# Kernel tuning notes

Hardware: AMD Instinct MI355X
Metric: run time of the kernel (lower is better)

The kernel has to match this reference:

```python
import jax, jax.numpy as jnp
import numpy as np

D_MODEL = 1024
NUM_HEADS = 4
KEY_DIM = 1024      # expand_k = 1
VALUE_DIM = 2048    # expand_v = 2
HEAD_QK = KEY_DIM // NUM_HEADS   # 256
HEAD_V = VALUE_DIM // NUM_HEADS  # 512
EPS = 1e-5
CHUNK = 64
ROPE_BASE = 10000.0


def apply_rotary(q, k):
    # q, k: (b, n, h, d), non-interleaved (rotate-half) rotary
    n, d = q.shape[1], q.shape[-1]
    inv_freq = 1.0 / (ROPE_BASE ** (jnp.arange(0, d, 2, dtype=jnp.float32) / d))
    t = jnp.arange(n, dtype=jnp.float32)
    freqs = jnp.outer(t, inv_freq)                     # (n, d/2)
    cos = jnp.cos(freqs)[None, :, None, :]
    sin = jnp.sin(freqs)[None, :, None, :]
    def rot(x):
        x1, x2 = jnp.split(x, 2, axis=-1)
        return jnp.concatenate([x1 * cos - x2 * sin, x2 * cos + x1 * sin], axis=-1)
    return rot(q), rot(k)


def chunk_retention(q, k, v, gamma, chunk=CHUNK):
    # q,k: (B,H,N,dk); v: (B,H,N,dv); gamma: (H,) per-head decay
    B, H, N, dk = q.shape
    dv = v.shape[-1]
    NC = N // chunk
    # (NC, B, H, C, d) chunked layout for scan
    qc = jnp.moveaxis(q.reshape(B, H, NC, chunk, dk), 2, 0)
    kc = jnp.moveaxis(k.reshape(B, H, NC, chunk, dk), 2, 0)
    vc = jnp.moveaxis(v.reshape(B, H, NC, chunk, dv), 2, 0)

    idx = jnp.arange(chunk)
    rel = idx[:, None] - idx[None, :]                       # i - j
    # intra-chunk decay mask D[h,i,j] = gamma_h**(i-j) for i>=j else 0
    D = jnp.where(rel >= 0, gamma[:, None, None] ** rel, 0.0)       # (H,C,C)
    cross_q = (gamma[:, None] ** (idx + 1))[None, :, :, None]       # (1,H,C,1)
    cross_k = (gamma[:, None] ** (chunk - 1 - idx))[None, :, :, None]
    gC = (gamma ** chunk)[None, :, None, None]                      # (1,H,1,1)

    def step(S, qkv):
        qb, kb, vb = qkv                                    # (B,H,C,d)
        attn = jnp.einsum('bhid,bhjd->bhij', qb, kb) * D[None]
        o_intra = jnp.einsum('bhij,bhjd->bhid', attn, vb)
        o_inter = jnp.einsum('bhid,bhde->bhie', qb * cross_q, S)
        S_new = gC * S + jnp.einsum('bhjd,bhje->bhde', kb * cross_k, vb)
        return S_new, o_intra + o_inter

    S0 = jnp.zeros((B, H, dk, dv), dtype=q.dtype)
    _, o = jax.lax.scan(step, S0, (qc, kc, vc))             # (NC,B,H,C,dv)
    return jnp.moveaxis(o, 0, 2).reshape(B, H, N, dv)


def rmsnorm(x, w):
    var = jnp.mean(x * x, axis=-1, keepdims=True)
    return x * jax.lax.rsqrt(var + EPS) * w


def setup_inputs() -> dict:
    key = jax.random.key(0)
    ks = jax.random.split(key, 7)
    B, N = 2, 4096
    s = 0.02
    return {
        'x': jax.random.normal(ks[0], (B, N, D_MODEL), dtype=jnp.float32),
        'Wq': jax.random.normal(ks[1], (D_MODEL, D_MODEL), dtype=jnp.float32) * s,
        'Wk': jax.random.normal(ks[2], (D_MODEL, D_MODEL), dtype=jnp.float32) * s,
        'Wv': jax.random.normal(ks[3], (D_MODEL, VALUE_DIM), dtype=jnp.float32) * s,
        'Wg': jax.random.normal(ks[4], (D_MODEL, VALUE_DIM), dtype=jnp.float32) * s,
        'Wo': jax.random.normal(ks[5], (VALUE_DIM, D_MODEL), dtype=jnp.float32) * s,
        'gn_weight': jnp.ones((HEAD_V,), dtype=jnp.float32),
    }


def reference(x, Wq, Wk, Wv, Wg, Wo, gn_weight):
    B, N, _ = x.shape
    H = NUM_HEADS
    q1 = (x @ Wq).reshape(B, N, H, HEAD_QK)
    k1 = (x @ Wk).reshape(B, N, H, HEAD_QK)
    q1, k1 = apply_rotary(q1, k1)
    q = jnp.transpose(q1, (0, 2, 1, 3)) * (HEAD_QK ** -0.5)   # (B,H,N,dk)
    k = jnp.transpose(k1, (0, 2, 1, 3))
    v = jnp.transpose((x @ Wv).reshape(B, N, H, HEAD_V), (0, 2, 1, 3))
    gamma = 1.0 - jnp.exp2(-5.0 - jnp.arange(H, dtype=jnp.float32))
    o = chunk_retention(q, k, v, gamma)                       # (B,H,N,dv_h)
    o = jnp.transpose(o, (0, 2, 1, 3))                        # (B,N,H,dv_h)
    o = rmsnorm(o, gn_weight)
    g = jax.nn.silu(x @ Wg)                                   # (B,N,VALUE_DIM)
    o = o.reshape(B, N, VALUE_DIM) * g
    return o @ Wo
```

## Files before the change

kernel.cpp:

```cpp
#include <hip/hip_runtime.h>

#define NS   4096
#define NBAT 2
#define NH   4
#define DKH  256
#define DVH  512
#define DM   1024
#define VD   2048
#define CH   64
#define NCH  64

typedef unsigned short u16;
typedef unsigned int   u32;

using bf16x8 = __attribute__((ext_vector_type(8))) short;
using f32x4  = __attribute__((ext_vector_type(4))) float;

__device__ __forceinline__ float bf2f(u16 a) {
  return __uint_as_float(((u32)a) << 16);
}
__device__ __forceinline__ u16 f2bf(float f) {
  u32 u = __float_as_uint(f);
  u32 r = (u + 0x7fffu + ((u >> 16) & 1u)) >> 16;
  return (u16)r;
}
__device__ __forceinline__ void unpack2(u32 v, float& lo, float& hi) {
  lo = __uint_as_float(v << 16);
  hi = __uint_as_float(v & 0xffff0000u);
}
__device__ __forceinline__ void unpack8(uint4 v, float* f) {
  unpack2(v.x, f[0], f[1]); unpack2(v.y, f[2], f[3]);
  unpack2(v.z, f[4], f[5]); unpack2(v.w, f[6], f[7]);
}

__device__ __forceinline__ void gl_lds16(const u16* g, u16* l) {
  __builtin_amdgcn_global_load_lds(
      (const __attribute__((address_space(1))) void*)g,
      (__attribute__((address_space(3))) void*)l,
      16, 0, 0);
}

__global__ __launch_bounds__(256) void cvt_bf16(const float* __restrict__ X,
                                                u16* __restrict__ Y) {
  size_t t = (size_t)blockIdx.x * 256 + threadIdx.x;
  float4 v = *(const float4*)(X + t * 4);
  ushort4 o;
  o.x = f2bf(v.x); o.y = f2bf(v.y); o.z = f2bf(v.z); o.w = f2bf(v.w);
  *(ushort4*)(Y + t * 4) = o;
}

__global__ __launch_bounds__(256) void transpose_bf16(const float* __restrict__ W,
                                                      u16* __restrict__ Wt,
                                                      int K, int N) {
  __shared__ float tile[64][65];
  const int n0 = blockIdx.x * 64, k0 = blockIdx.y * 64;
  const int t = threadIdx.x;
  const int r = t >> 4, c = (t & 15) << 2;
#pragma unroll
  for (int it = 0; it < 4; it++) {
    float4 v = *(const float4*)(W + (size_t)(k0 + r + it * 16) * N + n0 + c);
    tile[r + it * 16][c + 0] = v.x; tile[r + it * 16][c + 1] = v.y;
    tile[r + it * 16][c + 2] = v.z; tile[r + it * 16][c + 3] = v.w;
  }
  __syncthreads();
#pragma unroll
  for (int it = 0; it < 4; it++) {
    const int nr = r + it * 16;
    ushort4 o;
    o.x = f2bf(tile[c + 0][nr]); o.y = f2bf(tile[c + 1][nr]);
    o.z = f2bf(tile[c + 2][nr]); o.w = f2bf(tile[c + 3][nr]);
    *(ushort4*)(Wt + (size_t)(n0 + nr) * K + k0 + c) = o;
  }
}

template<bool OBF>
__global__ __launch_bounds__(256) void gemm_mfma(const u16* __restrict__ A,
                                                 const u16* __restrict__ Bt,
                                                 void* __restrict__ C,
                                                 int M, int N, int K) {
  __shared__ u16 sA[128 * 64];
  __shared__ u16 sB[128 * 64];
  const int tid = threadIdx.x;
  const int wave = tid >> 6, lane = tid & 63;
  const int wm = (wave >> 1) << 6;
  const int wn = (wave & 1) << 6;
  const int row0 = blockIdx.y << 7, col0 = blockIdx.x << 7;

  const int srow = tid >> 3;
  const int sk   = (tid & 7) << 3;

  const u16* aRow = A + (size_t)(row0 + srow) * K + sk;
  const u16* bRow = Bt + (size_t)(col0 + srow) * K + sk;
  u16* sAp = sA + tid * 8;
  u16* sBp = sB + tid * 8;

  f32x4 acc[4][4] = {};

  const int fm = lane & 15;
  const int fk = (lane >> 4) << 3;
  const u16* sAf = sA + (wm + fm) * 64 + fk;
  const u16* sBf = sB + (wn + fm) * 64 + fk;

  for (int k0 = 0; k0 < K; k0 += 64) {
#pragma unroll
    for (int it = 0; it < 4; it++) {
      gl_lds16(aRow + (size_t)(it * 32) * K + k0, sAp + it * 2048);
      gl_lds16(bRow + (size_t)(it * 32) * K + k0, sBp + it * 2048);
    }
    __syncthreads();
#pragma unroll
    for (int kk = 0; kk < 64; kk += 32) {
      bf16x8 af[4], bfr[4];
#pragma unroll
      for (int mt = 0; mt < 4; mt++) af[mt] = *(const bf16x8*)(sAf + mt * 1024 + kk);
#pragma unroll
      for (int nt = 0; nt < 4; nt++) bfr[nt] = *(const bf16x8*)(sBf + nt * 1024 + kk);
#pragma unroll
      for (int mt = 0; mt < 4; mt++)
#pragma unroll
        for (int nt = 0; nt < 4; nt++)
          acc[mt][nt] = __builtin_amdgcn_mfma_f32_16x16x32_bf16(af[mt], bfr[nt], acc[mt][nt], 0, 0, 0);
    }
    __syncthreads();
  }

  const int er = lane >> 4;
  const int ec = lane & 15;
#pragma unroll
  for (int mt = 0; mt < 4; mt++) {
#pragma unroll
    for (int nt = 0; nt < 4; nt++) {
#pragma unroll
      for (int r = 0; r < 4; r++) {
        const size_t row = (size_t)row0 + wm + mt * 16 + er * 4 + r;
        const size_t col = (size_t)col0 + wn + nt * 16 + ec;
        if constexpr (OBF) ((u16*)C)[row * N + col] = f2bf(acc[mt][nt][r]);
        else               ((float*)C)[row * N + col] = acc[mt][nt][r];
      }
    }
  }
}

__global__ __launch_bounds__(256) void rope_kernel(u16* __restrict__ Q, u16* __restrict__ K) {
  size_t t = (size_t)blockIdx.x * 256 + threadIdx.x;
  int j = (int)(t & 127);
  int h = (int)((t >> 7) & 3);
  size_t bn = t >> 9;
  int n = (int)(bn & (NS - 1));
  float ang = (float)n * exp2f(-(float)j * (13.2877123795494f / 128.0f));
  float s, c;
  sincosf(ang, &s, &c);
  size_t base = bn * DM + (size_t)h * DKH + j;
  const float sc = 0.0625f;
  float q1 = bf2f(Q[base]), q2 = bf2f(Q[base + 128]);
  Q[base]       = f2bf((q1 * c - q2 * s) * sc);
  Q[base + 128] = f2bf((q2 * c + q1 * s) * sc);
  float k1 = bf2f(K[base]), k2 = bf2f(K[base + 128]);
  K[base]       = f2bf(k1 * c - k2 * s);
  K[base + 128] = f2bf(k2 * c + k1 * s);
}

__global__ __launch_bounds__(256) void transpose_k(const u16* __restrict__ Kb,
                                                   u16* __restrict__ KT) {
  __shared__ u16 tile[64][68];
  const int wg = blockIdx.x;
  const int dt = wg & 3, nt = (wg >> 2) & 63, h = (wg >> 8) & 3, b = wg >> 10;
  const int tid = threadIdx.x;
  const int r = tid >> 2, cb = (tid & 3) << 4;
  const u16* src = Kb + (size_t)(b * NS + nt * 64 + r) * DM + h * DKH + dt * 64 + cb;
  *(uint4*)&tile[r][cb]     = *(const uint4*)(src);
  *(uint4*)&tile[r][cb + 8] = *(const uint4*)(src + 8);
  __syncthreads();
  const int dr = tid >> 2, ncb = (tid & 3) << 4;
  u32 w[8];
#pragma unroll
  for (int u = 0; u < 8; u++)
    w[u] = (u32)tile[ncb + 2 * u][dr] | ((u32)tile[ncb + 2 * u + 1][dr] << 16);
  u16* dst = KT + ((size_t)((b * NH + h) * 256) + dt * 64 + dr) * NS + nt * 64 + ncb;
  *(uint4*)(dst)     = make_uint4(w[0], w[1], w[2], w[3]);
  *(uint4*)(dst + 8) = make_uint4(w[4], w[5], w[6], w[7]);
}

__global__ __launch_bounds__(256) void attn_mfma(const u16* __restrict__ Q,
                                                 const u16* __restrict__ Kb,
                                                 u16* __restrict__ At) {
  __shared__ u16 sQ[64][264];
  __shared__ u16 sK[64][264];
  const int wg = blockIdx.x;
  const int c = wg & 63, h = (wg >> 6) & 3, b = wg >> 8;
  const int n0 = c << 6;
  const int tid = threadIdx.x;
  const int wave = tid >> 6, lane = tid & 63;
  const int quad = lane >> 4, col = lane & 15;
  {
    const int r = tid >> 2, cb = (tid & 3) << 6;
    const u16* qsrc = Q  + (size_t)(b * NS + n0 + r) * DM + h * DKH + cb;
    const u16* ksrc = Kb + (size_t)(b * NS + n0 + r) * DM + h * DKH + cb;
#pragma unroll
    for (int u = 0; u < 8; u++) {
      *(uint4*)&sQ[r][cb + u * 8] = *(const uint4*)(qsrc + u * 8);
      *(uint4*)&sK[r][cb + u * 8] = *(const uint4*)(ksrc + u * 8);
    }
  }
  __syncthreads();
  const int i0 = wave << 4;
  f32x4 acc[4] = {};
#pragma unroll
  for (int ks = 0; ks < 256; ks += 32) {
    bf16x8 a = *(const bf16x8*)&sQ[i0 + col][ks + quad * 8];
#pragma unroll
    for (int nt = 0; nt < 4; nt++) {
      bf16x8 bb = *(const bf16x8*)&sK[nt * 16 + col][ks + quad * 8];
      acc[nt] = __builtin_amdgcn_mfma_f32_16x16x32_bf16(a, bb, acc[nt], 0, 0, 0);
    }
  }
  const float l2g = log2f(1.0f - exp2f(-5.0f - (float)h));
  u16* dst = At + ((size_t)wg << 12);
#pragma unroll
  for (int nt = 0; nt < 4; nt++) {
    int j = nt * 16 + col;
#pragma unroll
    for (int rr = 0; rr < 4; rr++) {
      int i = i0 + quad * 4 + rr;
      int rel = i - j;
      float v = (rel >= 0) ? acc[nt][rr] * exp2f((float)rel * l2g) : 0.0f;
      dst[i * 64 + j] = f2bf(v);
    }
  }
}

__global__ __launch_bounds__(256) void scan_mfma(const u16* __restrict__ Q,
                                                 const u16* __restrict__ KT,
                                                 const u16* __restrict__ At,
                                                 u16* V) {
  __shared__ u16 sQ[64][264];
  __shared__ u16 sKT[256][72];
  __shared__ u16 sAi[64][72];
  __shared__ u16 sVT[32][72];
  __shared__ u16 sVkT[32][72];
  __shared__ u16 sSb[32][264];

  const int wg = blockIdx.x;
  const int es = wg & 15, h = (wg >> 4) & 3, b = wg >> 6;
  const int tid = threadIdx.x;
  const int wave = tid >> 6, lane = tid & 63;
  const int quad = lane >> 4, col = lane & 15;

  const float gamma = 1.0f - exp2f(-5.0f - (float)h);
  const float l2g = log2f(gamma);
  const float gC = exp2f(64.0f * l2g);

  const int qr = tid >> 2, qc = (tid & 3) << 6;
  const int ar = tid >> 2, ac = (tid & 3) << 4;
  const int vj = tid >> 2, ve = (tid & 3) << 3;
  const float ckj = exp2f((float)(63 - vj) * l2g);

  const int i0 = wave << 4;
  const int d0w = wave << 6;
  const float cq_base = exp2f((float)(i0 + quad * 4 + 1) * l2g);

  const u16* Qbase  = Q + ((size_t)b * NS) * DM + h * DKH;
  const u16* KTbase = KT + ((size_t)(b * NH + h) * 256) * NS;
  const u16* Atbase = At + ((size_t)((b * NH + h) * NCH) << 12);
  u16* Vbase = V + ((size_t)b * NS) * VD + h * DVH + es * 32;

  f32x4 accU[4][2] = {};

  for (int ch = 0; ch < NCH; ch++) {
    const int n0 = ch << 6;
    {
      const u16* src = Qbase + (size_t)(n0 + qr) * DM + qc;
#pragma unroll
      for (int u = 0; u < 8; u++)
        *(uint4*)&sQ[qr][qc + u * 8] = *(const uint4*)(src + u * 8);
    }
#pragma unroll
    for (int u = 0; u < 8; u++) {
      int cc = u * 256 + tid;
      int d = cc >> 3, off = (cc & 7) << 3;
      *(uint4*)&sKT[d][off] = *(const uint4*)(KTbase + (size_t)d * NS + n0 + off);
    }
    {
      const u16* src = Atbase + ((size_t)ch << 12) + ar * 64 + ac;
      *(uint4*)&sAi[ar][ac]     = *(const uint4*)(src);
      *(uint4*)&sAi[ar][ac + 8] = *(const uint4*)(src + 8);
    }
    {
      uint4 vv = *(const uint4*)(Vbase + (size_t)(n0 + vj) * VD + ve);
      float vf[8]; unpack8(vv, vf);
      const u16* raw = (const u16*)&vv;
#pragma unroll
      for (int u = 0; u < 8; u++) {
        sVT[ve + u][vj]  = raw[u];
        sVkT[ve + u][vj] = f2bf(vf[u] * ckj);
      }
    }
    __syncthreads();

    {
      f32x4 ai[2] = {}, ae[2] = {};
#pragma unroll
      for (int ks = 0; ks < 64; ks += 32) {
        bf16x8 a = *(const bf16x8*)&sAi[i0 + col][ks + quad * 8];
#pragma unroll
        for (int nt = 0; nt < 2; nt++) {
          bf16x8 bb = *(const bf16x8*)&sVT[nt * 16 + col][ks + quad * 8];
          ai[nt] = __builtin_amdgcn_mfma_f32_16x16x32_bf16(a, bb, ai[nt], 0, 0, 0);
        }
      }
      if (ch) {
#pragma unroll
        for (int ks = 0; ks < 256; ks += 32) {
          bf16x8 a = *(const bf16x8*)&sQ[i0 + col][ks + quad * 8];
#pragma unroll
          for (int nt = 0; nt < 2; nt++) {
            bf16x8 bb = *(const bf16x8*)&sSb[nt * 16 + col][ks + quad * 8];
            ae[nt] = __builtin_amdgcn_mfma_f32_16x16x32_bf16(a, bb, ae[nt], 0, 0, 0);
          }
        }
      }
      float cq = cq_base;
#pragma unroll
      for (int r = 0; r < 4; r++) {
        int i = i0 + quad * 4 + r;
        u16* dst = Vbase + (size_t)(n0 + i) * VD + col;
#pragma unroll
        for (int nt = 0; nt < 2; nt++)
          dst[nt * 16] = f2bf(ai[nt][r] + cq * ae[nt][r]);
        cq *= gamma;
      }
    }

#pragma unroll
    for (int mt = 0; mt < 4; mt++)
#pragma unroll
      for (int nt = 0; nt < 2; nt++)
        accU[mt][nt] = accU[mt][nt] * gC;
#pragma unroll
    for (int ks = 0; ks < 64; ks += 32) {
      bf16x8 bb[2];
#pragma unroll
      for (int nt = 0; nt < 2; nt++)
        bb[nt] = *(const bf16x8*)&sVkT[nt * 16 + col][ks + quad * 8];
#pragma unroll
      for (int mt = 0; mt < 4; mt++) {
        bf16x8 a = *(const bf16x8*)&sKT[d0w + mt * 16 + col][ks + quad * 8];
#pragma unroll
        for (int nt = 0; nt < 2; nt++)
          accU[mt][nt] = __builtin_amdgcn_mfma_f32_16x16x32_bf16(a, bb[nt], accU[mt][nt], 0, 0, 0);
      }
    }
    __syncthreads();

#pragma unroll
    for (int mt = 0; mt < 4; mt++) {
      int d = d0w + mt * 16 + quad * 4;
#pragma unroll
      for (int nt = 0; nt < 2; nt++) {
        int e = nt * 16 + col;
#pragma unroll
        for (int r = 0; r < 4; r++)
          sSb[e][d + r] = f2bf(accU[mt][nt][r]);
      }
    }
  }
}

__global__ __launch_bounds__(256) void norm_gate_kernel(const u16* __restrict__ O,
                                                        const u16* __restrict__ G,
                                                        const float* __restrict__ gnw,
                                                        u16* __restrict__ OG) {
  const int bn = blockIdx.x;
  const int wave = threadIdx.x >> 6;
  const int lane = threadIdx.x & 63;
  const size_t base = (size_t)bn * VD + (size_t)wave * DVH;
  float vals[8];
  float ss = 0.f;
#pragma unroll
  for (int k = 0; k < 8; k++) {
    float v = bf2f(O[base + lane + 64 * k]);
    vals[k] = v;
    ss += v * v;
  }
#pragma unroll
  for (int off = 32; off > 0; off >>= 1) ss += __shfl_xor(ss, off, 64);
  const float r = rsqrtf(ss * (1.0f / 512.0f) + 1e-5f);
#pragma unroll
  for (int k = 0; k < 8; k++) {
    int e = lane + 64 * k;
    float g = bf2f(G[base + e]);
    float sig = 1.0f / (1.0f + expf(-g));
    OG[base + e] = f2bf(vals[k] * r * gnw[e] * g * sig);
  }
}

extern "C" void kernel_launch(void* const* d_in, const int* in_sizes, int n_in,
                              void* d_out, int out_size, void* d_ws, size_t ws_size,
                              hipStream_t stream) {
  const float* x   = (const float*)d_in[0];
  const float* Wq  = (const float*)d_in[1];
  const float* Wk  = (const float*)d_in[2];
  const float* Wv  = (const float*)d_in[3];
  const float* Wg  = (const float*)d_in[4];
  const float* Wo  = (const float*)d_in[5];
  const float* gnw = (const float*)d_in[6];

  char* ws = (char*)d_ws;
  u16*   xb  = (u16*)(ws);
  u16*   Qb  = (u16*)(ws + (16u  << 20));
  u16*   Kb  = (u16*)(ws + (32u  << 20));
  u16*   Vb  = (u16*)(ws + (48u  << 20));
  u16*   Gb  = (u16*)(ws + (80u  << 20));
  u16*   At  = (u16*)(ws + (112u << 20));
  u16*   KTg = (u16*)(ws + (116u << 20));
  u16*   Wqt = (u16*)(ws + (132u << 20));
  u16*   Wkt = (u16*)(ws + (134u << 20));
  u16*   Wvt = (u16*)(ws + (136u << 20));
  u16*   Wgt = (u16*)(ws + (140u << 20));
  u16*   Wot = (u16*)(ws + (144u << 20));
  u16*   OG  = (u16*)(ws);

  dim3 blk(256);
  const int M = NBAT * NS;

  cvt_bf16<<<8192, blk, 0, stream>>>(x, xb);
  transpose_bf16<<<dim3(16, 16), blk, 0, stream>>>(Wq, Wqt, DM, DM);
  transpose_bf16<<<dim3(16, 16), blk, 0, stream>>>(Wk, Wkt, DM, DM);
  transpose_bf16<<<dim3(32, 16), blk, 0, stream>>>(Wv, Wvt, DM, VD);
  transpose_bf16<<<dim3(32, 16), blk, 0, stream>>>(Wg, Wgt, DM, VD);
  transpose_bf16<<<dim3(16, 32), blk, 0, stream>>>(Wo, Wot, VD, DM);

  gemm_mfma<true><<<dim3(8, 64),  blk, 0, stream>>>(xb, Wqt, Qb, M, DM, DM);
  gemm_mfma<true><<<dim3(8, 64),  blk, 0, stream>>>(xb, Wkt, Kb, M, DM, DM);
  gemm_mfma<true><<<dim3(16, 64), blk, 0, stream>>>(xb, Wvt, Vb, M, VD, DM);
  gemm_mfma<true><<<dim3(16, 64), blk, 0, stream>>>(xb, Wgt, Gb, M, VD, DM);

  rope_kernel<<<16384, blk, 0, stream>>>(Qb, Kb);
  transpose_k<<<2048, blk, 0, stream>>>(Kb, KTg);
  attn_mfma<<<512, blk, 0, stream>>>(Qb, Kb, At);
  scan_mfma<<<128, blk, 0, stream>>>(Qb, KTg, At, Vb);
  norm_gate_kernel<<<M, blk, 0, stream>>>(Vb, Gb, gnw, OG);

  gemm_mfma<false><<<dim3(8, 64), blk, 0, stream>>>(OG, Wot, (float*)d_out, M, DM, VD);
}
```

Before: 593.9 us.

## Split scan into output/state warp roles with register-prefetched chunk operands

The retention scan kernel is reorganized: value columns per block are halved so twice as many blocks launch, each with 512 threads, where four waves compute chunk outputs and four waves update the recurrent state. Q, intra-chunk attention and K^T tiles are loaded straight into registers and double-buffered for the next chunk instead of being staged through shared memory, which cuts LDS usage and overlaps global loads with MFMA work. This targets the low parallelism of the serial 64-chunk scan (only 128 blocks before) at the cost of more register pressure and duplicated Q/K loads across twice as many blocks.

Measured after the change: 550.8 us. 7.3% less time.

```diff
diff --git a/kernel.cpp b/kernel.cpp
--- a/kernel.cpp
+++ b/kernel.cpp
@@ -229,19 +229,16 @@
   }
 }
 
-__global__ __launch_bounds__(256) void scan_mfma(const u16* __restrict__ Q,
-                                                 const u16* __restrict__ KT,
-                                                 const u16* __restrict__ At,
-                                                 u16* V) {
-  __shared__ u16 sQ[64][264];
-  __shared__ u16 sKT[256][72];
-  __shared__ u16 sAi[64][72];
-  __shared__ u16 sVT[32][72];
-  __shared__ u16 sVkT[32][72];
-  __shared__ u16 sSb[32][264];
+__global__ __launch_bounds__(512, 2) void scan_mfma(const u16* __restrict__ Q,
+                                                    const u16* __restrict__ KT,
+                                                    const u16* __restrict__ At,
+                                                    u16* V) {
+  __shared__ u16 sVT[16][72];
+  __shared__ u16 sVkT[16][72];
+  __shared__ u16 sSb[16][264];
 
   const int wg = blockIdx.x;
-  const int es = wg & 15, h = (wg >> 4) & 3, b = wg >> 6;
+  const int es = wg & 31, h = (wg >> 5) & 3, b = wg >> 7;
   const int tid = threadIdx.x;
   const int wave = tid >> 6, lane = tid & 63;
   const int quad = lane >> 4, col = lane & 15;
@@ -250,45 +247,48 @@
   const float l2g = log2f(gamma);
   const float gC = exp2f(64.0f * l2g);
 
-  const int qr = tid >> 2, qc = (tid & 3) << 6;
-  const int ar = tid >> 2, ac = (tid & 3) << 4;
-  const int vj = tid >> 2, ve = (tid & 3) << 3;
+  const bool isO = wave < 4;
+  const int i0  = (wave & 3) << 4;
+  const int d0w = (wave & 3) << 6;
+  const float cq0 = exp2f((float)(i0 + quad * 4 + 1) * l2g);
+
+  const u16* Qb2 = Q  + (size_t)b * NS * DM + h * DKH;
+  const u16* KTb = KT + (size_t)((b * NH + h) * 256) * NS;
+  const u16* Atb = At + ((size_t)((b * NH + h) * NCH) << 12);
+  u16* Vb2 = V + (size_t)b * NS * VD + h * DVH + es * 16;
+
+  const int vj = (tid & 127) >> 1, ve = (tid & 1) << 3;
   const float ckj = exp2f((float)(63 - vj) * l2g);
 
-  const int i0 = wave << 4;
-  const int d0w = wave << 6;
-  const float cq_base = exp2f((float)(i0 + quad * 4 + 1) * l2g);
-
-  const u16* Qbase  = Q + ((size_t)b * NS) * DM + h * DKH;
-  const u16* KTbase = KT + ((size_t)(b * NH + h) * 256) * NS;
-  const u16* Atbase = At + ((size_t)((b * NH + h) * NCH) << 12);
-  u16* Vbase = V + ((size_t)b * NS) * VD + h * DVH + es * 32;
-
-  f32x4 accU[4][2] = {};
-
+  bf16x8 qf[2][8], af[2][2], kf[2][8];
+  uint4 vv[2];
+
+  if (tid < 128) vv[0] = *(const uint4*)(Vb2 + (size_t)vj * VD + ve);
+  if (isO) {
+    const u16* qrow = Qb2 + (size_t)(i0 + col) * DM + quad * 8;
+#pragma unroll
+    for (int k = 0; k < 8; k++) qf[0][k] = *(const bf16x8*)(qrow + k * 32);
+    const u16* arow = Atb + (i0 + col) * 64 + quad * 8;
+    af[0][0] = *(const bf16x8*)(arow);
+    af[0][1] = *(const bf16x8*)(arow + 32);
+  } else {
+#pragma unroll
+    for (int mt = 0; mt < 4; mt++) {
+      const u16* krow = KTb + (size_t)(d0w + mt * 16 + col) * NS + quad * 8;
+      kf[0][mt * 2]     = *(const bf16x8*)(krow);
+      kf[0][mt * 2 + 1] = *(const bf16x8*)(krow + 32);
+    }
+  }
+
+  f32x4 accU[4] = {};
+
+#pragma unroll 2
   for (int ch = 0; ch < NCH; ch++) {
+    const int cur = ch & 1, nxt = cur ^ 1;
     const int n0 = ch << 6;
-    {
-      const u16* src = Qbase + (size_t)(n0 + qr) * DM + qc;
-#pragma unroll
-      for (int u = 0; u < 8; u++)
-        *(uint4*)&sQ[qr][qc + u * 8] = *(const uint4*)(src + u * 8);
-    }
-#pragma unroll
-    for (int u = 0; u < 8; u++) {
-      int cc = u * 256 + tid;
-      int d = cc >> 3, off = (cc & 7) << 3;
-      *(uint4*)&sKT[d][off] = *(const uint4*)(KTbase + (size_t)d * NS + n0 + off);
-    }
-    {
-      const u16* src = Atbase + ((size_t)ch << 12) + ar * 64 + ac;
-      *(uint4*)&sAi[ar][ac]     = *(const uint4*)(src);
-      *(uint4*)&sAi[ar][ac + 8] = *(const uint4*)(src + 8);
-    }
-    {
-      uint4 vv = *(const uint4*)(Vbase + (size_t)(n0 + vj) * VD + ve);
-      float vf[8]; unpack8(vv, vf);
-      const u16* raw = (const u16*)&vv;
+    if (tid < 128) {
+      float vf[8]; unpack8(vv[cur], vf);
+      const u16* raw = (const u16*)&vv[cur];
 #pragma unroll
       for (int u = 0; u < 8; u++) {
         sVT[ve + u][vj]  = raw[u];
@@ -296,71 +296,65 @@
       }
     }
     __syncthreads();
-
-    {
-      f32x4 ai[2] = {}, ae[2] = {};
-#pragma unroll
-      for (int ks = 0; ks < 64; ks += 32) {
-        bf16x8 a = *(const bf16x8*)&sAi[i0 + col][ks + quad * 8];
-#pragma unroll
-        for (int nt = 0; nt < 2; nt++) {
-          bf16x8 bb = *(const bf16x8*)&sVT[nt * 16 + col][ks + quad * 8];
-          ai[nt] = __builtin_amdgcn_mfma_f32_16x16x32_bf16(a, bb, ai[nt], 0, 0, 0);
+    if (ch + 1 < NCH) {
+      const int n1 = n0 + 64;
+      if (tid < 128) vv[nxt] = *(const uint4*)(Vb2 + (size_t)(n1 + vj) * VD + ve);
+      if (isO) {
+        const u16* qrow = Qb2 + (size_t)(n1 + i0 + col) * DM + quad * 8;
+#pragma unroll
+        for (int k = 0; k < 8; k++) qf[nxt][k] = *(const bf16x8*)(qrow + k * 32);
+        const u16* arow = Atb + ((size_t)(ch + 1) << 12) + (i0 + col) * 64 + quad * 8;
+        af[nxt][0] = *(const bf16x8*)(arow);
+        af[nxt][1] = *(const bf16x8*)(arow + 32);
+      } else {
+#pragma unroll
+        for (int mt = 0; mt < 4; mt++) {
+          const u16* krow = KTb + (size_t)(d0w + mt * 16 + col) * NS + n1 + quad * 8;
+          kf[nxt][mt * 2]     = *(const bf16x8*)(krow);
+          kf[nxt][mt * 2 + 1] = *(const bf16x8*)(krow + 32);
         }
       }
+    }
+    if (isO) {
+      f32x4 ai = {}, ae = {};
+#pragma unroll
+      for (int k = 0; k < 2; k++) {
+        bf16x8 bb = *(const bf16x8*)&sVT[col][k * 32 + quad * 8];
+        ai = __builtin_amdgcn_mfma_f32_16x16x32_bf16(af[cur][k], bb, ai, 0, 0, 0);
+      }
       if (ch) {
 #pragma unroll
-        for (int ks = 0; ks < 256; ks += 32) {
-          bf16x8 a = *(const bf16x8*)&sQ[i0 + col][ks + quad * 8];
-#pragma unroll
-          for (int nt = 0; nt < 2; nt++) {
-            bf16x8 bb = *(const bf16x8*)&sSb[nt * 16 + col][ks + quad * 8];
-            ae[nt] = __builtin_amdgcn_mfma_f32_16x16x32_bf16(a, bb, ae[nt], 0, 0, 0);
-          }
+        for (int k = 0; k < 8; k++) {
+          bf16x8 bb = *(const bf16x8*)&sSb[col][k * 32 + quad * 8];
+          ae = __builtin_amdgcn_mfma_f32_16x16x32_bf16(qf[cur][k], bb, ae, 0, 0, 0);
         }
       }
-      float cq = cq_base;
+      float cq = cq0;
 #pragma unroll
       for (int r = 0; r < 4; r++) {
-        int i = i0 + quad * 4 + r;
-        u16* dst = Vbase + (size_t)(n0 + i) * VD + col;
-#pragma unroll
-        for (int nt = 0; nt < 2; nt++)
-          dst[nt * 16] = f2bf(ai[nt][r] + cq * ae[nt][r]);
+        u16* dst = Vb2 + (size_t)(n0 + i0 + quad * 4 + r) * VD + col;
+        *dst = f2bf(ai[r] + cq * ae[r]);
         cq *= gamma;
       }
-    }
-
-#pragma unroll
-    for (int mt = 0; mt < 4; mt++)
-#pragma unroll
-      for (int nt = 0; nt < 2; nt++)
-        accU[mt][nt] = accU[mt][nt] * gC;
-#pragma unroll
-    for (int ks = 0; ks < 64; ks += 32) {
-      bf16x8 bb[2];
-#pragma unroll
-      for (int nt = 0; nt < 2; nt++)
-        bb[nt] = *(const bf16x8*)&sVkT[nt * 16 + col][ks + quad * 8];
+    } else {
+#pragma unroll
+      for (int mt = 0; mt < 4; mt++) accU[mt] *= gC;
+#pragma unroll
+      for (int k = 0; k < 2; k++) {
+        bf16x8 bb = *(const bf16x8*)&sVkT[col][k * 32 + quad * 8];
+#pragma unroll
+        for (int mt = 0; mt < 4; mt++)
+          accU[mt] = __builtin_amdgcn_mfma_f32_16x16x32_bf16(kf[cur][mt * 2 + k], bb, accU[mt], 0, 0, 0);
+      }
+    }
+    __syncthreads();
+    if (!isO) {
 #pragma unroll
       for (int mt = 0; mt < 4; mt++) {
-        bf16x8 a = *(const bf16x8*)&sKT[d0w + mt * 16 + col][ks + quad * 8];
-#pragma unroll
-        for (int nt = 0; nt < 2; nt++)
-          accU[mt][nt] = __builtin_amdgcn_mfma_f32_16x16x32_bf16(a, bb[nt], accU[mt][nt], 0, 0, 0);
-      }
-    }
-    __syncthreads();
-
-#pragma unroll
-    for (int mt = 0; mt < 4; mt++) {
-      int d = d0w + mt * 16 + quad * 4;
-#pragma unroll
-      for (int nt = 0; nt < 2; nt++) {
-        int e = nt * 16 + col;
+        int d = d0w + mt * 16 + quad * 4;
 #pragma unroll
         for (int r = 0; r < 4; r++)
-          sSb[e][d + r] = f2bf(accU[mt][nt][r]);
+          sSb[col][d + r] = f2bf(accU[mt][r]);
       }
     }
   }
@@ -438,7 +432,7 @@
   rope_kernel<<<16384, blk, 0, stream>>>(Qb, Kb);
   transpose_k<<<2048, blk, 0, stream>>>(Kb, KTg);
   attn_mfma<<<512, blk, 0, stream>>>(Qb, Kb, At);
-  scan_mfma<<<128, blk, 0, stream>>>(Qb, KTg, At, Vb);
+  scan_mfma<<<256, dim3(512), 0, stream>>>(Qb, KTg, At, Vb);
   norm_gate_kernel<<<M, blk, 0, stream>>>(Vb, Gb, gnw, OG);
 
   gemm_mfma<false><<<dim3(8, 64), blk, 0, stream>>>(OG, Wot, (float*)d_out, M, DM, VD);
```

## Split chunk retention scan into parallel state pass and segmented output pass

Applied to the files above, without the earlier changes.

Replaces the single 128-block sequential scan with two kernels. A state pass computes inter-chunk states every 8 chunks across many small wavefront blocks. An output pass then processes 8 segments in parallel per head, seeded from those checkpoints, keeping the state in registers and using a 16x16x16 MFMA for the Q·S product. The V projection GEMM now writes V transposed so both passes read it directly. This targets the low parallelism of the serial scan, at the cost of extra state recompute, global checkpoint traffic, heavy register use, and uncoalesced global loads without LDS staging.

After: 668.8 us. +12.6%, slower.

```diff
diff --git a/kernel.cpp b/kernel.cpp
--- a/kernel.cpp
+++ b/kernel.cpp
@@ -9,11 +9,13 @@
 #define VD   2048
 #define CH   64
 #define NCH  64
+#define MROW (NBAT * NS)
 
 typedef unsigned short u16;
 typedef unsigned int   u32;
 
 using bf16x8 = __attribute__((ext_vector_type(8))) short;
+using bf16x4 = __attribute__((ext_vector_type(4))) short;
 using f32x4  = __attribute__((ext_vector_type(4))) float;
 
 __device__ __forceinline__ float bf2f(u16 a) {
@@ -38,6 +40,38 @@
       (const __attribute__((address_space(1))) void*)g,
       (__attribute__((address_space(3))) void*)l,
       16, 0, 0);
+}
+
+__device__ __forceinline__ f32x4 mfma32(bf16x8 a, bf16x8 b, f32x4 c) {
+  return __builtin_amdgcn_mfma_f32_16x16x32_bf16(a, b, c, 0, 0, 0);
+}
+
+__device__ __forceinline__ f32x4 mfma16(bf16x4 a, bf16x4 b, f32x4 c) {
+#if __has_builtin(__builtin_amdgcn_mfma_f32_16x16x16bf16_1k)
+  return __builtin_amdgcn_mfma_f32_16x16x16bf16_1k(a, b, c, 0, 0, 0);
+#else
+  asm("v_mfma_f32_16x16x16_bf16 %0, %1, %2, %0" : "+v"(c) : "v"(a), "v"(b));
+  return c;
+#endif
+}
+
+__device__ __forceinline__ bf16x8 scale8(bf16x8 v, const float* ckv) {
+  u32* w = (u32*)&v;
+  bf16x8 out;
+  u32* ow = (u32*)&out;
+#pragma unroll
+  for (int p = 0; p < 4; p++) {
+    float lo, hi; unpack2(w[p], lo, hi);
+    ow[p] = (u32)f2bf(lo * ckv[2 * p]) | ((u32)f2bf(hi * ckv[2 * p + 1]) << 16);
+  }
+  return out;
+}
+
+__device__ __forceinline__ bf16x4 pack4(f32x4 v) {
+  bf16x4 o;
+  o[0] = (short)f2bf(v[0]); o[1] = (short)f2bf(v[1]);
+  o[2] = (short)f2bf(v[2]); o[3] = (short)f2bf(v[3]);
+  return o;
 }
 
 __global__ __launch_bounds__(256) void cvt_bf16(const float* __restrict__ X,
@@ -73,7 +107,7 @@
   }
 }
 
-template<bool OBF>
+template<int OMODE>
 __global__ __launch_bounds__(256) void gemm_mfma(const u16* __restrict__ A,
                                                  const u16* __restrict__ Bt,
                                                  void* __restrict__ C,
@@ -119,7 +153,7 @@
       for (int mt = 0; mt < 4; mt++)
 #pragma unroll
         for (int nt = 0; nt < 4; nt++)
-          acc[mt][nt] = __builtin_amdgcn_mfma_f32_16x16x32_bf16(af[mt], bfr[nt], acc[mt][nt], 0, 0, 0);
+          acc[mt][nt] = mfma32(af[mt], bfr[nt], acc[mt][nt]);
     }
     __syncthreads();
   }
@@ -130,12 +164,21 @@
   for (int mt = 0; mt < 4; mt++) {
 #pragma unroll
     for (int nt = 0; nt < 4; nt++) {
-#pragma unroll
-      for (int r = 0; r < 4; r++) {
-        const size_t row = (size_t)row0 + wm + mt * 16 + er * 4 + r;
-        const size_t col = (size_t)col0 + wn + nt * 16 + ec;
-        if constexpr (OBF) ((u16*)C)[row * N + col] = f2bf(acc[mt][nt][r]);
-        else               ((float*)C)[row * N + col] = acc[mt][nt][r];
+      if constexpr (OMODE == 2) {
+        ushort4 o;
+        o.x = f2bf(acc[mt][nt][0]); o.y = f2bf(acc[mt][nt][1]);
+        o.z = f2bf(acc[mt][nt][2]); o.w = f2bf(acc[mt][nt][3]);
+        u16* dst = (u16*)C + (size_t)(col0 + wn + nt * 16 + ec) * M +
+                   row0 + wm + mt * 16 + er * 4;
+        *(ushort4*)dst = o;
+      } else {
+#pragma unroll
+        for (int r = 0; r < 4; r++) {
+          const size_t row = (size_t)row0 + wm + mt * 16 + er * 4 + r;
+          const size_t col = (size_t)col0 + wn + nt * 16 + ec;
+          if constexpr (OMODE == 1) ((u16*)C)[row * N + col] = f2bf(acc[mt][nt][r]);
+          else                      ((float*)C)[row * N + col] = acc[mt][nt][r];
+        }
       }
     }
   }
@@ -211,7 +254,7 @@
 #pragma unroll
     for (int nt = 0; nt < 4; nt++) {
       bf16x8 bb = *(const bf16x8*)&sK[nt * 16 + col][ks + quad * 8];
-      acc[nt] = __builtin_amdgcn_mfma_f32_16x16x32_bf16(a, bb, acc[nt], 0, 0, 0);
+      acc[nt] = mfma32(a, bb, acc[nt]);
     }
   }
   const float l2g = log2f(1.0f - exp2f(-5.0f - (float)h));
@@ -229,139 +272,192 @@
   }
 }
 
-__global__ __launch_bounds__(256) void scan_mfma(const u16* __restrict__ Q,
-                                                 const u16* __restrict__ KT,
-                                                 const u16* __restrict__ At,
-                                                 u16* V) {
-  __shared__ u16 sQ[64][264];
-  __shared__ u16 sKT[256][72];
-  __shared__ u16 sAi[64][72];
-  __shared__ u16 sVT[32][72];
-  __shared__ u16 sVkT[32][72];
-  __shared__ u16 sSb[32][264];
-
+__global__ __launch_bounds__(64) void state_pass(const u16* __restrict__ KT,
+                                                 const u16* __restrict__ VT,
+                                                 u16* __restrict__ Sc) {
   const int wg = blockIdx.x;
-  const int es = wg & 15, h = (wg >> 4) & 3, b = wg >> 6;
-  const int tid = threadIdx.x;
-  const int wave = tid >> 6, lane = tid & 63;
+  const int bh = wg & 7, slice = wg >> 3;
+  const int ds = slice & 7, es = slice >> 3;
+  const int b = bh >> 2, h = bh & 3;
+  const int lane = threadIdx.x;
   const int quad = lane >> 4, col = lane & 15;
-
   const float gamma = 1.0f - exp2f(-5.0f - (float)h);
   const float l2g = log2f(gamma);
   const float gC = exp2f(64.0f * l2g);
-
-  const int qr = tid >> 2, qc = (tid & 3) << 6;
-  const int ar = tid >> 2, ac = (tid & 3) << 4;
-  const int vj = tid >> 2, ve = (tid & 3) << 3;
-  const float ckj = exp2f((float)(63 - vj) * l2g);
-
-  const int i0 = wave << 4;
-  const int d0w = wave << 6;
-  const float cq_base = exp2f((float)(i0 + quad * 4 + 1) * l2g);
-
-  const u16* Qbase  = Q + ((size_t)b * NS) * DM + h * DKH;
-  const u16* KTbase = KT + ((size_t)(b * NH + h) * 256) * NS;
-  const u16* Atbase = At + ((size_t)((b * NH + h) * NCH) << 12);
-  u16* Vbase = V + ((size_t)b * NS) * VD + h * DVH + es * 32;
-
-  f32x4 accU[4][2] = {};
-
+  float ck[2][8];
+#pragma unroll
+  for (int ks = 0; ks < 2; ks++)
+#pragma unroll
+    for (int u = 0; u < 8; u++)
+      ck[ks][u] = exp2f((float)(63 - (ks * 32 + quad * 8 + u)) * l2g);
+
+  const u16* KTb = KT + (size_t)(bh * 256 + ds * 32) * NS;
+  const u16* vrow = VT + (size_t)(h * DVH + es * 16 + col) * MROW + (size_t)b * NS;
+
+  f32x4 S[2] = {};
+  bf16x8 kf[2][4], vf[2][2];
+
+#pragma unroll
+  for (int mt = 0; mt < 2; mt++)
+#pragma unroll
+    for (int ks = 0; ks < 2; ks++)
+      kf[0][mt * 2 + ks] = *(const bf16x8*)(KTb + (size_t)(mt * 16 + col) * NS + ks * 32 + quad * 8);
+#pragma unroll
+  for (int ks = 0; ks < 2; ks++)
+    vf[0][ks] = *(const bf16x8*)(vrow + ks * 32 + quad * 8);
+
+#pragma unroll 2
   for (int ch = 0; ch < NCH; ch++) {
+    const int cur = ch & 1, nxt = cur ^ 1;
+    if (ch + 1 < NCH) {
+      const int n1 = (ch + 1) << 6;
+#pragma unroll
+      for (int mt = 0; mt < 2; mt++)
+#pragma unroll
+        for (int ks = 0; ks < 2; ks++)
+          kf[nxt][mt * 2 + ks] = *(const bf16x8*)(KTb + (size_t)(mt * 16 + col) * NS + n1 + ks * 32 + quad * 8);
+#pragma unroll
+      for (int ks = 0; ks < 2; ks++)
+        vf[nxt][ks] = *(const bf16x8*)(vrow + n1 + ks * 32 + quad * 8);
+    }
+#pragma unroll
+    for (int mt = 0; mt < 2; mt++) S[mt] *= gC;
+#pragma unroll
+    for (int ks = 0; ks < 2; ks++) {
+      bf16x8 ckv = scale8(vf[cur][ks], ck[ks]);
+#pragma unroll
+      for (int mt = 0; mt < 2; mt++)
+        S[mt] = mfma32(kf[cur][mt * 2 + ks], ckv, S[mt]);
+    }
+    if ((ch & 7) == 7 && ch != NCH - 1) {
+      const int sidx = ch >> 3;
+      u16* sp = Sc + (size_t)((bh * 7 + sidx) * 512 + es * 16 + col) * 256 + ds * 32;
+#pragma unroll
+      for (int mt = 0; mt < 2; mt++) {
+        ushort4 o;
+        o.x = f2bf(S[mt][0]); o.y = f2bf(S[mt][1]);
+        o.z = f2bf(S[mt][2]); o.w = f2bf(S[mt][3]);
+        *(ushort4*)(sp + mt * 16 + quad * 4) = o;
+      }
+    }
+  }
+}
+
+__global__ __launch_bounds__(64, 1) void out_pass(const u16* __restrict__ Q,
+                                                  const u16* __restrict__ KT,
+                                                  const u16* __restrict__ At,
+                                                  const u16* __restrict__ VT,
+                                                  const u16* __restrict__ Sc,
+                                                  u16* __restrict__ O) {
+  const int wg = blockIdx.x;
+  const int grp = wg & 63, es = wg >> 6;
+  const int sc = grp & 7, bh = grp >> 3;
+  const int b = bh >> 2, h = bh & 3;
+  const int lane = threadIdx.x;
+  const int quad = lane >> 4, col = lane & 15;
+  const float gamma = 1.0f - exp2f(-5.0f - (float)h);
+  const float l2g = log2f(gamma);
+  const float gC = exp2f(64.0f * l2g);
+  const float g16 = exp2f(16.0f * l2g);
+  const float cq00 = exp2f((float)(quad * 4 + 1) * l2g);
+  float ck[2][8];
+#pragma unroll
+  for (int ks = 0; ks < 2; ks++)
+#pragma unroll
+    for (int u = 0; u < 8; u++)
+      ck[ks][u] = exp2f((float)(63 - (ks * 32 + quad * 8 + u)) * l2g);
+
+  const u16* Qb  = Q + (size_t)(b * NS) * DM + h * DKH;
+  const u16* KTb = KT + (size_t)(bh * 256) * NS;
+  const u16* Atb = At + ((size_t)(bh * NCH) << 12);
+  const u16* vrow0 = VT + (size_t)(h * DVH + es * 32 + col) * MROW + (size_t)b * NS;
+  const u16* vrow1 = vrow0 + (size_t)16 * MROW;
+  u16* Ob = O + (size_t)(b * NS) * VD + h * DVH + es * 32;
+
+  f32x4 S[2][16];
+  bf16x4 SB[2][16];
+  if (sc) {
+    const u16* sp0 = Sc + (size_t)((bh * 7 + sc - 1) * 512 + es * 32 + col) * 256;
+    const u16* sp1 = sp0 + (size_t)16 * 256;
+#pragma unroll
+    for (int mt = 0; mt < 16; mt++) {
+      ushort4 w0 = *(const ushort4*)(sp0 + mt * 16 + quad * 4);
+      ushort4 w1 = *(const ushort4*)(sp1 + mt * 16 + quad * 4);
+      SB[0][mt][0] = (short)w0.x; SB[0][mt][1] = (short)w0.y;
+      SB[0][mt][2] = (short)w0.z; SB[0][mt][3] = (short)w0.w;
+      SB[1][mt][0] = (short)w1.x; SB[1][mt][1] = (short)w1.y;
+      SB[1][mt][2] = (short)w1.z; SB[1][mt][3] = (short)w1.w;
+      S[0][mt] = f32x4{bf2f(w0.x), bf2f(w0.y), bf2f(w0.z), bf2f(w0.w)};
+      S[1][mt] = f32x4{bf2f(w1.x), bf2f(w1.y), bf2f(w1.z), bf2f(w1.w)};
+    }
+  } else {
+#pragma unroll
+    for (int nt = 0; nt < 2; nt++)
+#pragma unroll
+      for (int mt = 0; mt < 16; mt++) { S[nt][mt] = f32x4{0.f, 0.f, 0.f, 0.f}; SB[nt][mt] = bf16x4{0, 0, 0, 0}; }
+  }
+
+  for (int c = 0; c < 8; c++) {
+    const int ch = sc * 8 + c;
     const int n0 = ch << 6;
-    {
-      const u16* src = Qbase + (size_t)(n0 + qr) * DM + qc;
-#pragma unroll
-      for (int u = 0; u < 8; u++)
-        *(uint4*)&sQ[qr][qc + u * 8] = *(const uint4*)(src + u * 8);
-    }
-#pragma unroll
-    for (int u = 0; u < 8; u++) {
-      int cc = u * 256 + tid;
-      int d = cc >> 3, off = (cc & 7) << 3;
-      *(uint4*)&sKT[d][off] = *(const uint4*)(KTbase + (size_t)d * NS + n0 + off);
-    }
-    {
-      const u16* src = Atbase + ((size_t)ch << 12) + ar * 64 + ac;
-      *(uint4*)&sAi[ar][ac]     = *(const uint4*)(src);
-      *(uint4*)&sAi[ar][ac + 8] = *(const uint4*)(src + 8);
-    }
-    {
-      uint4 vv = *(const uint4*)(Vbase + (size_t)(n0 + vj) * VD + ve);
-      float vf[8]; unpack8(vv, vf);
-      const u16* raw = (const u16*)&vv;
-#pragma unroll
-      for (int u = 0; u < 8; u++) {
-        sVT[ve + u][vj]  = raw[u];
-        sVkT[ve + u][vj] = f2bf(vf[u] * ckj);
+    f32x4 ai[4][2] = {}, ae[4][2] = {};
+    bf16x8 vfr[2][2];
+#pragma unroll
+    for (int ks = 0; ks < 2; ks++) {
+      vfr[ks][0] = *(const bf16x8*)(vrow0 + n0 + ks * 32 + quad * 8);
+      vfr[ks][1] = *(const bf16x8*)(vrow1 + n0 + ks * 32 + quad * 8);
+#pragma unroll
+      for (int mt = 0; mt < 4; mt++) {
+        bf16x8 a = *(const bf16x8*)(Atb + ((size_t)ch << 12) + (mt * 16 + col) * 64 + ks * 32 + quad * 8);
+        ai[mt][0] = mfma32(a, vfr[ks][0], ai[mt][0]);
+        ai[mt][1] = mfma32(a, vfr[ks][1], ai[mt][1]);
       }
     }
-    __syncthreads();
-
-    {
-      f32x4 ai[2] = {}, ae[2] = {};
-#pragma unroll
-      for (int ks = 0; ks < 64; ks += 32) {
-        bf16x8 a = *(const bf16x8*)&sAi[i0 + col][ks + quad * 8];
-#pragma unroll
-        for (int nt = 0; nt < 2; nt++) {
-          bf16x8 bb = *(const bf16x8*)&sVT[nt * 16 + col][ks + quad * 8];
-          ai[nt] = __builtin_amdgcn_mfma_f32_16x16x32_bf16(a, bb, ai[nt], 0, 0, 0);
+    if (sc || c) {
+#pragma unroll
+      for (int kt = 0; kt < 16; kt++) {
+#pragma unroll
+        for (int mt = 0; mt < 4; mt++) {
+          ushort4 qa = *(const ushort4*)(Qb + (size_t)(n0 + mt * 16 + col) * DM + kt * 16 + quad * 4);
+          bf16x4 a; a[0] = (short)qa.x; a[1] = (short)qa.y; a[2] = (short)qa.z; a[3] = (short)qa.w;
+          ae[mt][0] = mfma16(a, SB[0][kt], ae[mt][0]);
+          ae[mt][1] = mfma16(a, SB[1][kt], ae[mt][1]);
         }
       }
-      if (ch) {
-#pragma unroll
-        for (int ks = 0; ks < 256; ks += 32) {
-          bf16x8 a = *(const bf16x8*)&sQ[i0 + col][ks + quad * 8];
-#pragma unroll
-          for (int nt = 0; nt < 2; nt++) {
-            bf16x8 bb = *(const bf16x8*)&sSb[nt * 16 + col][ks + quad * 8];
-            ae[nt] = __builtin_amdgcn_mfma_f32_16x16x32_bf16(a, bb, ae[nt], 0, 0, 0);
-          }
+    }
+    float cqr = cq00;
+#pragma unroll
+    for (int mt = 0; mt < 4; mt++) {
+      float cq = cqr;
+#pragma unroll
+      for (int r = 0; r < 4; r++) {
+        u16* dst = Ob + (size_t)(n0 + mt * 16 + quad * 4 + r) * VD;
+        dst[col]      = f2bf(ai[mt][0][r] + cq * ae[mt][0][r]);
+        dst[16 + col] = f2bf(ai[mt][1][r] + cq * ae[mt][1][r]);
+        cq *= gamma;
+      }
+      cqr *= g16;
+    }
+    if (c < 7) {
+#pragma unroll
+      for (int nt = 0; nt < 2; nt++)
+#pragma unroll
+        for (int mt = 0; mt < 16; mt++) S[nt][mt] *= gC;
+#pragma unroll
+      for (int ks = 0; ks < 2; ks++) {
+        bf16x8 ckv0 = scale8(vfr[ks][0], ck[ks]);
+        bf16x8 ckv1 = scale8(vfr[ks][1], ck[ks]);
+#pragma unroll
+        for (int mt = 0; mt < 16; mt++) {
+          bf16x8 a = *(const bf16x8*)(KTb + (size_t)(mt * 16 + col) * NS + n0 + ks * 32 + quad * 8);
+          S[0][mt] = mfma32(a, ckv0, S[0][mt]);
+          S[1][mt] = mfma32(a, ckv1, S[1][mt]);
         }
       }
-      float cq = cq_base;
-#pragma unroll
-      for (int r = 0; r < 4; r++) {
-        int i = i0 + quad * 4 + r;
-        u16* dst = Vbase + (size_t)(n0 + i) * VD + col;
-#pragma unroll
-        for (int nt = 0; nt < 2; nt++)
-          dst[nt * 16] = f2bf(ai[nt][r] + cq * ae[nt][r]);
-        cq *= gamma;
-      }
-    }
-
-#pragma unroll
-    for (int mt = 0; mt < 4; mt++)
 #pragma unroll
       for (int nt = 0; nt < 2; nt++)
-        accU[mt][nt] = accU[mt][nt] * gC;
-#pragma unroll
-    for (int ks = 0; ks < 64; ks += 32) {
-      bf16x8 bb[2];
-#pragma unroll
-      for (int nt = 0; nt < 2; nt++)
-        bb[nt] = *(const bf16x8*)&sVkT[nt * 16 + col][ks + quad * 8];
-#pragma unroll
-      for (int mt = 0; mt < 4; mt++) {
-        bf16x8 a = *(const bf16x8*)&sKT[d0w + mt * 16 + col][ks + quad * 8];
-#pragma unroll
-        for (int nt = 0; nt < 2; nt++)
-          accU[mt][nt] = __builtin_amdgcn_mfma_f32_16x16x32_bf16(a, bb[nt], accU[mt][nt], 0, 0, 0);
-      }
-    }
-    __syncthreads();
-
-#pragma unroll
-    for (int mt = 0; mt < 4; mt++) {
-      int d = d0w + mt * 16 + quad * 4;
-#pragma unroll
-      for (int nt = 0; nt < 2; nt++) {
-        int e = nt * 16 + col;
-#pragma unroll
-        for (int r = 0; r < 4; r++)
-          sSb[e][d + r] = f2bf(accU[mt][nt][r]);
-      }
+#pragma unroll
+        for (int mt = 0; mt < 16; mt++) SB[nt][mt] = pack4(S[nt][mt]);
     }
   }
 }
@@ -407,9 +503,10 @@
 
   char* ws = (char*)d_ws;
   u16*   xb  = (u16*)(ws);
+  u16*   Sc  = (u16*)(ws);
   u16*   Qb  = (u16*)(ws + (16u  << 20));
   u16*   Kb  = (u16*)(ws + (32u  << 20));
-  u16*   Vb  = (u16*)(ws + (48u  << 20));
+  u16*   VT  = (u16*)(ws + (48u  << 20));
   u16*   Gb  = (u16*)(ws + (80u  << 20));
   u16*   At  = (u16*)(ws + (112u << 20));
   u16*   KTg = (u16*)(ws + (116u << 20));
@@ -418,10 +515,11 @@
   u16*   Wvt = (u16*)(ws + (136u << 20));
   u16*   Wgt = (u16*)(ws + (140u << 20));
   u16*   Wot = (u16*)(ws + (144u << 20));
+  u16*   Ob  = (u16*)(ws + (148u << 20));
   u16*   OG  = (u16*)(ws);
 
   dim3 blk(256);
-  const int M = NBAT * NS;
+  const int M = MROW;
 
   cvt_bf16<<<8192, blk, 0, stream>>>(x, xb);
   transpose_bf16<<<dim3(16, 16), blk, 0, stream>>>(Wq, Wqt, DM, DM);
@@ -430,16 +528,18 @@
   transpose_bf16<<<dim3(32, 16), blk, 0, stream>>>(Wg, Wgt, DM, VD);
   transpose_bf16<<<dim3(16, 32), blk, 0, stream>>>(Wo, Wot, VD, DM);
 
-  gemm_mfma<true><<<dim3(8, 64),  blk, 0, stream>>>(xb, Wqt, Qb, M, DM, DM);
-  gemm_mfma<true><<<dim3(8, 64),  blk, 0, stream>>>(xb, Wkt, Kb, M, DM, DM);
-  gemm_mfma<true><<<dim3(16, 64), blk, 0, stream>>>(xb, Wvt, Vb, M, VD, DM);
-  gemm_mfma<true><<<dim3(16, 64), blk, 0, stream>>>(xb, Wgt, Gb, M, VD, DM);
+  gemm_mfma<1><<<dim3(8, 64),  blk, 0, stream>>>(xb, Wqt, Qb, M, DM, DM);
+  gemm_mfma<1><<<dim3(8, 64),  blk, 0, stream>>>(xb, Wkt, Kb, M, DM, DM);
+  gemm_mfma<2><<<dim3(16, 64), blk, 0, stream>>>(xb, Wvt, VT, M, VD, DM);
+  gemm_mfma<1><<<dim3(16, 64), blk, 0, stream>>>(xb, Wgt, Gb, M, VD, DM);
 
   rope_kernel<<<16384, blk, 0, stream>>>(Qb, Kb);
   transpose_k<<<2048, blk, 0, stream>>>(Kb, KTg);
   attn_mfma<<<512, blk, 0, stream>>>(Qb, Kb, At);
-  scan_mfma<<<128, blk, 0, stream>>>(Qb, KTg, At, Vb);
-  norm_gate_kernel<<<M, blk, 0, stream>>>(Vb, Gb, gnw, OG);
-
-  gemm_mfma<false><<<dim3(8, 64), blk, 0, stream>>>(OG, Wot, (float*)d_out, M, DM, VD);
-}
+
+  state_pass<<<2048, dim3(64), 0, stream>>>(KTg, VT, Sc);
+  out_pass<<<1024, dim3(64), 0, stream>>>(Qb, KTg, At, VT, Sc, Ob);
+
+  norm_gate_kernel<<<M, blk, 0, stream>>>(Ob, Gb, gnw, OG);
+  gemm_mfma<0><<<dim3(8, 64), blk, 0, stream>>>(OG, Wot, (float*)d_out, M, DM, VD);
+}
```
